# Kernel tuning notes

Hardware: AMD Instinct MI355X
Metric: run time of the kernel (lower is better)

Reference implementation:

```python
import jax, jax.numpy as jnp
import numpy as np

NUM_CLASSES = 19  # configer.get('data','num_classes')


def _batch_label_vector(targets, num_classes, grid_size):
    # targets: [B, H, W] int labels in [0, num_classes)
    b, h, w = targets.shape
    pad_h = (-h) % grid_size
    pad_w = (-w) % grid_size
    # pad with value == num_classes, which torch.histc(min=0, max=num_classes-1)
    # ignores; we route it to an extra dustbin column and drop it.
    t = jnp.pad(targets, ((0, 0), (0, pad_h), (0, pad_w)),
                constant_values=num_classes)
    hh, ww = h + pad_h, w + pad_w
    # tile into (grid_size x grid_size) blocks -> [n_blocks, g*g]
    t = t.reshape(b, hh // grid_size, grid_size, ww // grid_size, grid_size)
    t = t.transpose(0, 1, 3, 2, 4).reshape(-1, grid_size * grid_size)
    n_blocks = t.shape[0]
    rows = jnp.arange(n_blocks)[:, None]  # [n_blocks, 1]
    # presence vector: hist > 0 <=> scatter-set ones at (block, label)
    tvect = jnp.zeros((n_blocks, num_classes + 1), jnp.float32)
    tvect = tvect.at[rows, t].set(1.0)
    return tvect[:, :num_classes]  # drop dustbin (pad value) column


def setup_inputs() -> dict:
    key = jax.random.key(0)
    k1, k2 = jax.random.split(key)
    B, H, W, G = 16, 1024, 2048, 8
    n_blocks = B * (H // G) * (W // G)  # 524288
    preds = jax.random.normal(k1, (n_blocks, NUM_CLASSES), jnp.float32)
    targets = jax.random.randint(k2, (B, H, W), 0, NUM_CLASSES, jnp.int32)
    return {"preds": preds, "targets": targets, "grid_size": G}


def reference(preds, targets, grid_size):
    se_target = _batch_label_vector(targets, NUM_CLASSES, grid_size)
    # BCELoss(sigmoid(preds), se_target), mean reduction.
    # Numerically stable: -log(sigmoid(x)) = softplus(-x),
    #                     -log(1-sigmoid(x)) = softplus(x)
    loss = se_target * jax.nn.softplus(-preds) + (1.0 - se_target) * jax.nn.softplus(preds)
    return jnp.mean(loss)
```

## Files before the change

kernel.cpp:

```cpp
#include <hip/hip_runtime.h>
#include <cmath>


typedef int   i4v __attribute__((ext_vector_type(4), aligned(16)));
typedef float f4u __attribute__((ext_vector_type(4), aligned(4)));

__global__ __launch_bounds__(256) void fsenc_loss_kernel(
    const float* __restrict__ preds,
    const int*   __restrict__ targets,
    float*       __restrict__ out,
    float inv_count)
{
    const int t    = threadIdx.x;
    const int band = blockIdx.x;

    const i4v* tb = (const i4v*)targets + (long)band * 4096;
    i4v tv[16];
    #pragma unroll
    for (int r = 0; r < 8; ++r) {
        tv[2*r]   = __builtin_nontemporal_load(tb + r * 512 + 2*t);
        tv[2*r+1] = __builtin_nontemporal_load(tb + r * 512 + 2*t + 1);
    }

    const float* p = preds + ((long)band * 256 + t) * 19;
    f4u q0 = __builtin_nontemporal_load((const f4u*)(p + 0));
    f4u q1 = __builtin_nontemporal_load((const f4u*)(p + 4));
    f4u q2 = __builtin_nontemporal_load((const f4u*)(p + 8));
    f4u q3 = __builtin_nontemporal_load((const f4u*)(p + 12));
    f4u q4 = __builtin_nontemporal_load((const f4u*)(p + 15));

    unsigned m = 0u;
    #pragma unroll
    for (int i = 0; i < 16; ++i) {
        i4v u = tv[i];
        m |= (1u << u[0]) | (1u << u[1]) | (1u << u[2]) | (1u << u[3]);
    }

    float acc = 0.f;
    #define SP_TERM(xval, cls)                                                 \
        {                                                                      \
            float x_ = (xval);                                                 \
            float sp_ = fmaxf(x_, 0.f) + __logf(1.f + __expf(-fabsf(x_)));     \
            acc += sp_ - (float)((m >> (cls)) & 1u) * x_;                      \
        }
    SP_TERM(q0[0], 0)  SP_TERM(q0[1], 1)  SP_TERM(q0[2], 2)  SP_TERM(q0[3], 3)
    SP_TERM(q1[0], 4)  SP_TERM(q1[1], 5)  SP_TERM(q1[2], 6)  SP_TERM(q1[3], 7)
    SP_TERM(q2[0], 8)  SP_TERM(q2[1], 9)  SP_TERM(q2[2], 10) SP_TERM(q2[3], 11)
    SP_TERM(q3[0], 12) SP_TERM(q3[1], 13) SP_TERM(q3[2], 14) SP_TERM(q3[3], 15)
    SP_TERM(q4[1], 16) SP_TERM(q4[2], 17) SP_TERM(q4[3], 18)
    #undef SP_TERM

    #pragma unroll
    for (int off = 32; off; off >>= 1)
        acc += __shfl_down(acc, off);

    __shared__ float s_part[4];
    if ((t & 63) == 0) s_part[t >> 6] = acc;
    __syncthreads();
    if (t == 0) {
        float tot = s_part[0] + s_part[1] + s_part[2] + s_part[3];
        atomicAdd(out, tot * inv_count);
    }
}

extern "C" void kernel_launch(void* const* d_in, const int* in_sizes, int n_in,
                              void* d_out, int out_size, void* d_ws, size_t ws_size,
                              hipStream_t stream) {
    const float* preds   = (const float*)d_in[0];
    const int*   targets = (const int*)d_in[1];
    float*       out     = (float*)d_out;

    const int B = 16, H = 1024;
    const float inv_count = 1.0f / (float)in_sizes[0];

    (void)hipMemsetAsync(out, 0, sizeof(float), stream);

    const int grid = B * (H / 8);
    fsenc_loss_kernel<<<grid, 256, 0, stream>>>(preds, targets, out, inv_count);
}
```

Measured before the change: 214.8 us.

## Coalesce preds loads and share per-block label masks through LDS

Each thread used to read its own block's 19 preds with unaligned, strided float4 loads. Now the block's preds band is read as contiguous aligned float4 vectors across threads, so every load instruction is fully coalesced. The target loads are also rearranged so adjacent threads read adjacent vectors. Each block's label-presence mask is built by a thread pair combined with a shuffle, then written to shared memory. The cost is an extra __syncthreads, a shared-memory lookup with a divide-by-19 index per element, and a divergent tail for threads that load a fifth vector.

```diff
diff --git a/kernel.cpp b/kernel.cpp
--- a/kernel.cpp
+++ b/kernel.cpp
@@ -3,7 +3,7 @@
 
 
 typedef int   i4v __attribute__((ext_vector_type(4), aligned(16)));
-typedef float f4u __attribute__((ext_vector_type(4), aligned(4)));
+typedef float f4v __attribute__((ext_vector_type(4), aligned(16)));
 
 __global__ __launch_bounds__(256) void fsenc_loss_kernel(
     const float* __restrict__ preds,
@@ -15,39 +15,60 @@
     const int band = blockIdx.x;
 
     const i4v* tb = (const i4v*)targets + (long)band * 4096;
-    i4v tv[16];
+    i4v ta[8], tc[8];
     #pragma unroll
     for (int r = 0; r < 8; ++r) {
-        tv[2*r]   = __builtin_nontemporal_load(tb + r * 512 + 2*t);
-        tv[2*r+1] = __builtin_nontemporal_load(tb + r * 512 + 2*t + 1);
+        ta[r] = __builtin_nontemporal_load(tb + r * 512 + t);
+        tc[r] = __builtin_nontemporal_load(tb + r * 512 + 256 + t);
     }
 
-    const float* p = preds + ((long)band * 256 + t) * 19;
-    f4u q0 = __builtin_nontemporal_load((const f4u*)(p + 0));
-    f4u q1 = __builtin_nontemporal_load((const f4u*)(p + 4));
-    f4u q2 = __builtin_nontemporal_load((const f4u*)(p + 8));
-    f4u q3 = __builtin_nontemporal_load((const f4u*)(p + 12));
-    f4u q4 = __builtin_nontemporal_load((const f4u*)(p + 15));
+    const f4v* pb = (const f4v*)preds + (long)band * 1216;
+    f4v q[5];
+    #pragma unroll
+    for (int k = 0; k < 4; ++k)
+        q[k] = __builtin_nontemporal_load(pb + t + 256 * k);
+    const bool has5 = (t < 192);
+    if (has5) q[4] = __builtin_nontemporal_load(pb + t + 1024);
 
-    unsigned m = 0u;
+    unsigned mA = 0u, mB = 0u;
     #pragma unroll
-    for (int i = 0; i < 16; ++i) {
-        i4v u = tv[i];
-        m |= (1u << u[0]) | (1u << u[1]) | (1u << u[2]) | (1u << u[3]);
+    for (int r = 0; r < 8; ++r) {
+        i4v u = ta[r];
+        mA |= (1u << u[0]) | (1u << u[1]) | (1u << u[2]) | (1u << u[3]);
+        i4v v = tc[r];
+        mB |= (1u << v[0]) | (1u << v[1]) | (1u << v[2]) | (1u << v[3]);
     }
+    mA |= __shfl_xor(mA, 1);
+    mB |= __shfl_xor(mB, 1);
+
+    __shared__ unsigned s_mask[256];
+    if ((t & 1) == 0) {
+        s_mask[t >> 1]         = mA;
+        s_mask[128 + (t >> 1)] = mB;
+    }
+    __syncthreads();
 
     float acc = 0.f;
-    #define SP_TERM(xval, cls)                                                 \
+    #define SP_TERM(xval, gidx)                                                \
         {                                                                      \
             float x_ = (xval);                                                 \
+            unsigned g_ = (unsigned)(gidx);                                    \
+            unsigned blk_ = g_ / 19u;                                          \
+            unsigned cls_ = g_ - blk_ * 19u;                                   \
             float sp_ = fmaxf(x_, 0.f) + __logf(1.f + __expf(-fabsf(x_)));     \
-            acc += sp_ - (float)((m >> (cls)) & 1u) * x_;                      \
+            acc += sp_ - (float)((s_mask[blk_] >> cls_) & 1u) * x_;            \
         }
-    SP_TERM(q0[0], 0)  SP_TERM(q0[1], 1)  SP_TERM(q0[2], 2)  SP_TERM(q0[3], 3)
-    SP_TERM(q1[0], 4)  SP_TERM(q1[1], 5)  SP_TERM(q1[2], 6)  SP_TERM(q1[3], 7)
-    SP_TERM(q2[0], 8)  SP_TERM(q2[1], 9)  SP_TERM(q2[2], 10) SP_TERM(q2[3], 11)
-    SP_TERM(q3[0], 12) SP_TERM(q3[1], 13) SP_TERM(q3[2], 14) SP_TERM(q3[3], 15)
-    SP_TERM(q4[1], 16) SP_TERM(q4[2], 17) SP_TERM(q4[3], 18)
+    #pragma unroll
+    for (int k = 0; k < 4; ++k) {
+        int g0 = 4 * (t + 256 * k);
+        SP_TERM(q[k][0], g0)     SP_TERM(q[k][1], g0 + 1)
+        SP_TERM(q[k][2], g0 + 2) SP_TERM(q[k][3], g0 + 3)
+    }
+    if (has5) {
+        int g0 = 4 * (t + 1024);
+        SP_TERM(q[4][0], g0)     SP_TERM(q[4][1], g0 + 1)
+        SP_TERM(q[4][2], g0 + 2) SP_TERM(q[4][3], g0 + 3)
+    }
     #undef SP_TERM
 
     #pragma unroll
```

After: 213.0 us. About the same (-0.8%).
